# Kernel optimization log

Measured on AMD Instinct MI355X. Metric: run time of the kernel, lower is better.

## Reference

```python
import jax, jax.numpy as jnp
jax.config.update("jax_enable_x64", True)  # original computes in float64
import numpy as np

ALPHA = 0.01  # init kwarg


def setup_inputs() -> dict:
    key = jax.random.key(0)
    x = jax.random.normal(key, (8, 8192, 512), dtype=jnp.float32)
    return {"x": x}


def reference(x):
    # x: [B, T, C]
    _, t, _ = x.shape
    # powers = flip(arange(t)) = [t-1, t-2, ..., 0]
    powers = jnp.arange(t - 1, -1, -1, dtype=jnp.float64)
    base = jnp.power(1.0 - ALPHA, powers)          # (1-alpha)^(t-1-i), [T]
    divisor = base.reshape(1, t, 1)                # [1, T, 1]
    weights = base.at[1:].multiply(ALPHA).reshape(1, t, 1)
    out = jnp.cumsum(x.astype(jnp.float64) * weights, axis=1) / divisor
    return out.astype(x.dtype)
```

## Files before the change

### kernel.cpp

```cpp
#include <hip/hip_runtime.h>
#include <math.h>


namespace {
constexpr int B = 8;
constexpr int T = 8192;
constexpr int C = 512;
constexpr float ALPHA = 0.01f;
constexpr float DECAY = 1.0f - ALPHA;
constexpr int S4 = C / 4;
constexpr int TPB = S4;
constexpr int CHUNK = 64;
constexpr int K = T / CHUNK;
constexpr int W = 32;

typedef float f32x4 __attribute__((ext_vector_type(4)));

__device__ __forceinline__ void ema_step(float4& y, const float4 v) {
    y.x = DECAY * y.x + ALPHA * v.x;
    y.y = DECAY * y.y + ALPHA * v.y;
    y.z = DECAY * y.z + ALPHA * v.z;
    y.w = DECAY * y.w + ALPHA * v.w;
}
}

__global__ __launch_bounds__(TPB) void ema_ends(const float* __restrict__ x,
                                                float* __restrict__ ends) {
    const int k = blockIdx.x;
    const int b = blockIdx.y;
    const int tid = threadIdx.x;
    const float4* xp = reinterpret_cast<const float4*>(x) +
                       (size_t)(b * T + k * CHUNK) * S4 + tid;
    float4 y;
    if (k == 0) {
        y = xp[0];
    } else {
        y = make_float4(0.f, 0.f, 0.f, 0.f);
    }
#pragma unroll 8
    for (int t = 0; t < CHUNK; ++t) {
        float4 v = xp[(size_t)t * S4];
        ema_step(y, v);
    }
    reinterpret_cast<float4*>(ends)[(size_t)(b * K + k) * S4 + tid] = y;
}

__global__ __launch_bounds__(TPB) void ema_fold_apply(const float* __restrict__ x,
                                                      const float* __restrict__ ends,
                                                      float* __restrict__ out,
                                                      float dC) {
    const int k = blockIdx.x;
    const int b = blockIdx.y;
    const int tid = threadIdx.x;
    const size_t base4 = (size_t)(b * T + k * CHUNK) * S4 + tid;
    const float4* xp = reinterpret_cast<const float4*>(x) + base4;
    float4* op = reinterpret_cast<float4*>(out) + base4;

    float4 y;
    if (k == 0) {
        y = xp[0];
    } else {
        y = make_float4(0.f, 0.f, 0.f, 0.f);
        const float4* ep = reinterpret_cast<const float4*>(ends) +
                           (size_t)b * K * S4 + tid;
        int m0 = k - W;
        if (m0 < 0) m0 = 0;
#pragma unroll 8
        for (int m = m0; m < k; ++m) {
            float4 e = ep[(size_t)m * S4];
            y.x = dC * y.x + e.x;
            y.y = dC * y.y + e.y;
            y.z = dC * y.z + e.z;
            y.w = dC * y.w + e.w;
        }
    }
#pragma unroll 8
    for (int t = 0; t < CHUNK; ++t) {
        float4 v = xp[(size_t)t * S4];
        ema_step(y, v);
        __builtin_nontemporal_store(*reinterpret_cast<const f32x4*>(&y),
                                    reinterpret_cast<f32x4*>(op + (size_t)t * S4));
    }
}

__global__ __launch_bounds__(TPB) void ema_seq_kernel(const float* __restrict__ x,
                                                      float* __restrict__ out) {
    const int b = blockIdx.x;
    const int tid = threadIdx.x;
    const float4* xp = reinterpret_cast<const float4*>(x) + (size_t)b * T * S4 + tid;
    float4* op = reinterpret_cast<float4*>(out) + (size_t)b * T * S4 + tid;
    float4 y = xp[0];
    for (int t = 0; t < T; ++t) {
        float4 v = xp[(size_t)t * S4];
        ema_step(y, v);
        op[(size_t)t * S4] = y;
    }
}

extern "C" void kernel_launch(void* const* d_in, const int* in_sizes, int n_in,
                              void* d_out, int out_size, void* d_ws, size_t ws_size,
                              hipStream_t stream) {
    (void)in_sizes; (void)n_in; (void)out_size;
    const float* x = reinterpret_cast<const float*>(d_in[0]);
    float* out = reinterpret_cast<float*>(d_out);

    const size_t need = (size_t)B * K * C * sizeof(float);
    if (ws_size >= need) {
        float* ends = reinterpret_cast<float*>(d_ws);
        const float dC = (float)pow((double)DECAY, (double)CHUNK);
        ema_ends<<<dim3(K, B), dim3(TPB), 0, stream>>>(x, ends);
        ema_fold_apply<<<dim3(K, B), dim3(TPB), 0, stream>>>(x, ends, out, dC);
    } else {
        ema_seq_kernel<<<dim3(B), dim3(TPB), 0, stream>>>(x, out);
    }
}
```

Before: 250.8 us.

## Fuse chunk-ends and fold-apply into single pass with inter-block flag waits

```diff
diff --git a/kernel.cpp b/kernel.cpp
--- a/kernel.cpp
+++ b/kernel.cpp
@@ -13,6 +13,7 @@
 constexpr int CHUNK = 64;
 constexpr int K = T / CHUNK;
 constexpr int W = 32;
+constexpr int NFLAGS = K * B;
 
 typedef float f32x4 __attribute__((ext_vector_type(4)));
 
@@ -24,13 +25,21 @@
 }
 }
 
-__global__ __launch_bounds__(TPB) void ema_ends(const float* __restrict__ x,
-                                                float* __restrict__ ends) {
+__global__ __launch_bounds__(1024) void ema_zero_flags(unsigned int* flags) {
+    flags[threadIdx.x] = 0u;
+}
+
+__global__ __launch_bounds__(TPB) void ema_onepass(const float* __restrict__ x,
+                                                   float* __restrict__ out,
+                                                   float* __restrict__ ends,
+                                                   unsigned int* __restrict__ flags,
+                                                   float dC) {
     const int k = blockIdx.x;
     const int b = blockIdx.y;
     const int tid = threadIdx.x;
-    const float4* xp = reinterpret_cast<const float4*>(x) +
-                       (size_t)(b * T + k * CHUNK) * S4 + tid;
+    const size_t base4 = (size_t)(b * T + k * CHUNK) * S4 + tid;
+    const float4* xp = reinterpret_cast<const float4*>(x) + base4;
+
     float4 y;
     if (k == 0) {
         y = xp[0];
@@ -42,38 +51,42 @@
         float4 v = xp[(size_t)t * S4];
         ema_step(y, v);
     }
-    reinterpret_cast<float4*>(ends)[(size_t)(b * K + k) * S4 + tid] = y;
-}
 
-__global__ __launch_bounds__(TPB) void ema_fold_apply(const float* __restrict__ x,
-                                                      const float* __restrict__ ends,
-                                                      float* __restrict__ out,
-                                                      float dC) {
-    const int k = blockIdx.x;
-    const int b = blockIdx.y;
-    const int tid = threadIdx.x;
-    const size_t base4 = (size_t)(b * T + k * CHUNK) * S4 + tid;
-    const float4* xp = reinterpret_cast<const float4*>(x) + base4;
-    float4* op = reinterpret_cast<float4*>(out) + base4;
+    float4* ep = reinterpret_cast<float4*>(ends) + (size_t)b * K * S4;
+    ep[(size_t)k * S4 + tid] = y;
+    __threadfence();
+    __syncthreads();
+    if (tid == 0) {
+        __hip_atomic_store(&flags[b * K + k], 1u,
+                           __ATOMIC_RELEASE, __HIP_MEMORY_SCOPE_AGENT);
+    }
 
-    float4 y;
     if (k == 0) {
         y = xp[0];
     } else {
+        const int m0 = (k > W) ? (k - W) : 0;
+        const int cnt = k - m0;
+        if (tid < cnt) {
+            while (__hip_atomic_load(&flags[b * K + m0 + tid],
+                                     __ATOMIC_RELAXED,
+                                     __HIP_MEMORY_SCOPE_AGENT) == 0u) {
+                __builtin_amdgcn_s_sleep(8);
+            }
+        }
+        __syncthreads();
+        __threadfence();
         y = make_float4(0.f, 0.f, 0.f, 0.f);
-        const float4* ep = reinterpret_cast<const float4*>(ends) +
-                           (size_t)b * K * S4 + tid;
-        int m0 = k - W;
-        if (m0 < 0) m0 = 0;
 #pragma unroll 8
         for (int m = m0; m < k; ++m) {
-            float4 e = ep[(size_t)m * S4];
+            float4 e = ep[(size_t)m * S4 + tid];
             y.x = dC * y.x + e.x;
             y.y = dC * y.y + e.y;
             y.z = dC * y.z + e.z;
             y.w = dC * y.w + e.w;
         }
     }
+
+    float4* op = reinterpret_cast<float4*>(out) + base4;
 #pragma unroll 8
     for (int t = 0; t < CHUNK; ++t) {
         float4 v = xp[(size_t)t * S4];
@@ -104,12 +117,16 @@
     const float* x = reinterpret_cast<const float*>(d_in[0]);
     float* out = reinterpret_cast<float*>(d_out);
 
-    const size_t need = (size_t)B * K * C * sizeof(float);
+    const size_t ends_bytes = (size_t)B * K * C * sizeof(float);
+    const size_t need = ends_bytes + NFLAGS * sizeof(unsigned int);
+
     if (ws_size >= need) {
         float* ends = reinterpret_cast<float*>(d_ws);
+        unsigned int* flags =
+            reinterpret_cast<unsigned int*>(reinterpret_cast<char*>(d_ws) + ends_bytes);
         const float dC = (float)pow((double)DECAY, (double)CHUNK);
-        ema_ends<<<dim3(K, B), dim3(TPB), 0, stream>>>(x, ends);
-        ema_fold_apply<<<dim3(K, B), dim3(TPB), 0, stream>>>(x, ends, out, dC);
+        ema_zero_flags<<<dim3(1), dim3(NFLAGS), 0, stream>>>(flags);
+        ema_onepass<<<dim3(K, B), dim3(TPB), 0, stream>>>(x, out, ends, flags, dC);
     } else {
         ema_seq_kernel<<<dim3(B), dim3(TPB), 0, stream>>>(x, out);
     }
```

After: 363.9 us. 1.45x slower.

## Break EMA dependency chains with weighted sums and double-buffered loads

Applied to the files above, without the earlier changes.

```diff
diff --git a/kernel.cpp b/kernel.cpp
--- a/kernel.cpp
+++ b/kernel.cpp
@@ -12,15 +12,28 @@
 constexpr int TPB = S4;
 constexpr int CHUNK = 64;
 constexpr int K = T / CHUNK;
-constexpr int W = 32;
+constexpr int W = 16;
 
 typedef float f32x4 __attribute__((ext_vector_type(4)));
+
+constexpr float dpow(int n) {
+    float r = 1.0f;
+    for (int i = 0; i < n; ++i) r *= DECAY;
+    return r;
+}
 
 __device__ __forceinline__ void ema_step(float4& y, const float4 v) {
     y.x = DECAY * y.x + ALPHA * v.x;
     y.y = DECAY * y.y + ALPHA * v.y;
     y.z = DECAY * y.z + ALPHA * v.z;
     y.w = DECAY * y.w + ALPHA * v.w;
+}
+
+__device__ __forceinline__ void wsum(float4& a, const float w, const float4 v) {
+    a.x += w * v.x;
+    a.y += w * v.y;
+    a.z += w * v.z;
+    a.w += w * v.w;
 }
 }
 
@@ -31,42 +44,74 @@
     const int tid = threadIdx.x;
     const float4* xp = reinterpret_cast<const float4*>(x) +
                        (size_t)(b * T + k * CHUNK) * S4 + tid;
+    float4 a0 = make_float4(0.f, 0.f, 0.f, 0.f);
+    float4 a1 = a0, a2 = a0, a3 = a0;
+    float4 x0;
+#pragma unroll
+    for (int t = 0; t < CHUNK; t += 4) {
+        float4 v0 = xp[(size_t)(t + 0) * S4];
+        float4 v1 = xp[(size_t)(t + 1) * S4];
+        float4 v2 = xp[(size_t)(t + 2) * S4];
+        float4 v3 = xp[(size_t)(t + 3) * S4];
+        if (t == 0) x0 = v0;
+        wsum(a0, ALPHA * dpow(CHUNK - 1 - (t + 0)), v0);
+        wsum(a1, ALPHA * dpow(CHUNK - 1 - (t + 1)), v1);
+        wsum(a2, ALPHA * dpow(CHUNK - 1 - (t + 2)), v2);
+        wsum(a3, ALPHA * dpow(CHUNK - 1 - (t + 3)), v3);
+    }
     float4 y;
+    y.x = (a0.x + a1.x) + (a2.x + a3.x);
+    y.y = (a0.y + a1.y) + (a2.y + a3.y);
+    y.z = (a0.z + a1.z) + (a2.z + a3.z);
+    y.w = (a0.w + a1.w) + (a2.w + a3.w);
     if (k == 0) {
-        y = xp[0];
-    } else {
-        y = make_float4(0.f, 0.f, 0.f, 0.f);
-    }
-#pragma unroll 8
-    for (int t = 0; t < CHUNK; ++t) {
-        float4 v = xp[(size_t)t * S4];
-        ema_step(y, v);
+        constexpr float e0 = (1.0f - ALPHA) * dpow(CHUNK - 1);
+        y.x += e0 * x0.x; y.y += e0 * x0.y; y.z += e0 * x0.z; y.w += e0 * x0.w;
     }
     reinterpret_cast<float4*>(ends)[(size_t)(b * K + k) * S4 + tid] = y;
 }
 
-__global__ __launch_bounds__(TPB) void ema_fold_apply(const float* __restrict__ x,
-                                                      const float* __restrict__ ends,
-                                                      float* __restrict__ out,
-                                                      float dC) {
+__global__ __launch_bounds__(TPB) void ema_apply(const float* __restrict__ x,
+                                                 const float* __restrict__ ends,
+                                                 float* __restrict__ out) {
     const int k = blockIdx.x;
     const int b = blockIdx.y;
     const int tid = threadIdx.x;
     const size_t base4 = (size_t)(b * T + k * CHUNK) * S4 + tid;
     const float4* xp = reinterpret_cast<const float4*>(x) + base4;
     float4* op = reinterpret_cast<float4*>(out) + base4;
+    const float4* ep = reinterpret_cast<const float4*>(ends) +
+                       (size_t)b * K * S4 + tid;
+
+    float4 buf[2][8];
+#pragma unroll
+    for (int i = 0; i < 8; ++i) buf[0][i] = xp[(size_t)i * S4];
 
     float4 y;
     if (k == 0) {
-        y = xp[0];
+        y = buf[0][0];
+    } else if (k > W) {
+        float4 c0 = make_float4(0.f, 0.f, 0.f, 0.f);
+        float4 c1 = c0, c2 = c0, c3 = c0;
+#pragma unroll
+        for (int j = 0; j < W; j += 4) {
+            float4 e0 = ep[(size_t)(k - 1 - (j + 0)) * S4];
+            float4 e1 = ep[(size_t)(k - 1 - (j + 1)) * S4];
+            float4 e2 = ep[(size_t)(k - 1 - (j + 2)) * S4];
+            float4 e3 = ep[(size_t)(k - 1 - (j + 3)) * S4];
+            wsum(c0, dpow(CHUNK * (j + 0)), e0);
+            wsum(c1, dpow(CHUNK * (j + 1)), e1);
+            wsum(c2, dpow(CHUNK * (j + 2)), e2);
+            wsum(c3, dpow(CHUNK * (j + 3)), e3);
+        }
+        y.x = (c0.x + c1.x) + (c2.x + c3.x);
+        y.y = (c0.y + c1.y) + (c2.y + c3.y);
+        y.z = (c0.z + c1.z) + (c2.z + c3.z);
+        y.w = (c0.w + c1.w) + (c2.w + c3.w);
     } else {
+        constexpr float dC = dpow(CHUNK);
         y = make_float4(0.f, 0.f, 0.f, 0.f);
-        const float4* ep = reinterpret_cast<const float4*>(ends) +
-                           (size_t)b * K * S4 + tid;
-        int m0 = k - W;
-        if (m0 < 0) m0 = 0;
-#pragma unroll 8
-        for (int m = m0; m < k; ++m) {
+        for (int m = 0; m < k; ++m) {
             float4 e = ep[(size_t)m * S4];
             y.x = dC * y.x + e.x;
             y.y = dC * y.y + e.y;
@@ -74,12 +119,22 @@
             y.w = dC * y.w + e.w;
         }
     }
-#pragma unroll 8
-    for (int t = 0; t < CHUNK; ++t) {
-        float4 v = xp[(size_t)t * S4];
-        ema_step(y, v);
-        __builtin_nontemporal_store(*reinterpret_cast<const f32x4*>(&y),
-                                    reinterpret_cast<f32x4*>(op + (size_t)t * S4));
+
+#pragma unroll
+    for (int g = 0; g < 8; ++g) {
+        const int cur = g & 1, nxt = cur ^ 1;
+        if (g < 7) {
+#pragma unroll
+            for (int i = 0; i < 8; ++i)
+                buf[nxt][i] = xp[(size_t)((g + 1) * 8 + i) * S4];
+        }
+#pragma unroll
+        for (int i = 0; i < 8; ++i) {
+            ema_step(y, buf[cur][i]);
+            __builtin_nontemporal_store(
+                *reinterpret_cast<const f32x4*>(&y),
+                reinterpret_cast<f32x4*>(op + (size_t)(g * 8 + i) * S4));
+        }
     }
 }
 
@@ -107,9 +162,8 @@
     const size_t need = (size_t)B * K * C * sizeof(float);
     if (ws_size >= need) {
         float* ends = reinterpret_cast<float*>(d_ws);
-        const float dC = (float)pow((double)DECAY, (double)CHUNK);
         ema_ends<<<dim3(K, B), dim3(TPB), 0, stream>>>(x, ends);
-        ema_fold_apply<<<dim3(K, B), dim3(TPB), 0, stream>>>(x, ends, out, dC);
+        ema_apply<<<dim3(K, B), dim3(TPB), 0, stream>>>(x, ends, out);
     } else {
         ema_seq_kernel<<<dim3(B), dim3(TPB), 0, stream>>>(x, out);
     }
```

After: 262.4 us. 1.05x slower.

## Fuse chunk-end and apply passes into one cooperative kernel with grid sync

Applied to the files above, without the earlier changes.

```diff
diff --git a/kernel.cpp b/kernel.cpp
--- a/kernel.cpp
+++ b/kernel.cpp
@@ -1,6 +1,9 @@
 #include <hip/hip_runtime.h>
+#include <hip/hip_cooperative_groups.h>
 #include <math.h>
 
+
+namespace cg = cooperative_groups;
 
 namespace {
 constexpr int B = 8;
@@ -12,9 +15,15 @@
 constexpr int TPB = S4;
 constexpr int CHUNK = 64;
 constexpr int K = T / CHUNK;
-constexpr int W = 32;
+constexpr int W = 16;
 
 typedef float f32x4 __attribute__((ext_vector_type(4)));
+
+constexpr float dpow(int n) {
+    float r = 1.0f;
+    for (int i = 0; i < n; ++i) r *= DECAY;
+    return r;
+}
 
 __device__ __forceinline__ void ema_step(float4& y, const float4 v) {
     y.x = DECAY * y.x + ALPHA * v.x;
@@ -22,7 +31,84 @@
     y.z = DECAY * y.z + ALPHA * v.z;
     y.w = DECAY * y.w + ALPHA * v.w;
 }
-}
+
+__device__ __forceinline__ void wsum(float4& a, const float w, const float4 v) {
+    a.x += w * v.x;
+    a.y += w * v.y;
+    a.z += w * v.z;
+    a.w += w * v.w;
+}
+}
+
+__global__ __launch_bounds__(TPB) void ema_fused(const float* __restrict__ x,
+                                                 float* __restrict__ out,
+                                                 float* __restrict__ ends) {
+    const int k = blockIdx.x;
+    const int b = blockIdx.y;
+    const int tid = threadIdx.x;
+    const size_t base4 = (size_t)(b * T + k * CHUNK) * S4 + tid;
+    const float4* xp = reinterpret_cast<const float4*>(x) + base4;
+    float4* ep = reinterpret_cast<float4*>(ends) + (size_t)b * K * S4 + tid;
+
+    float4 y;
+    if (k == 0) {
+        y = xp[0];
+    } else {
+        y = make_float4(0.f, 0.f, 0.f, 0.f);
+    }
+#pragma unroll 8
+    for (int t = 0; t < CHUNK; ++t) {
+        float4 v = xp[(size_t)t * S4];
+        ema_step(y, v);
+    }
+    ep[(size_t)k * S4] = y;
+
+    __threadfence();
+    cg::this_grid().sync();
+    __threadfence();
+
+    if (k == 0) {
+        y = xp[0];
+    } else if (k > W) {
+        float4 c0 = make_float4(0.f, 0.f, 0.f, 0.f);
+        float4 c1 = c0, c2 = c0, c3 = c0;
+#pragma unroll
+        for (int j = 0; j < W; j += 4) {
+            float4 e0 = ep[(size_t)(k - 1 - (j + 0)) * S4];
+            float4 e1 = ep[(size_t)(k - 1 - (j + 1)) * S4];
+            float4 e2 = ep[(size_t)(k - 1 - (j + 2)) * S4];
+            float4 e3 = ep[(size_t)(k - 1 - (j + 3)) * S4];
+            wsum(c0, dpow(CHUNK * (j + 0)), e0);
+            wsum(c1, dpow(CHUNK * (j + 1)), e1);
+            wsum(c2, dpow(CHUNK * (j + 2)), e2);
+            wsum(c3, dpow(CHUNK * (j + 3)), e3);
+        }
+        y.x = (c0.x + c1.x) + (c2.x + c3.x);
+        y.y = (c0.y + c1.y) + (c2.y + c3.y);
+        y.z = (c0.z + c1.z) + (c2.z + c3.z);
+        y.w = (c0.w + c1.w) + (c2.w + c3.w);
+    } else {
+        constexpr float dC = dpow(CHUNK);
+        y = make_float4(0.f, 0.f, 0.f, 0.f);
+        for (int m = 0; m < k; ++m) {
+            float4 e = ep[(size_t)m * S4];
+            y.x = dC * y.x + e.x;
+            y.y = dC * y.y + e.y;
+            y.z = dC * y.z + e.z;
+            y.w = dC * y.w + e.w;
+        }
+    }
+
+    float4* op = reinterpret_cast<float4*>(out) + base4;
+#pragma unroll 8
+    for (int t = 0; t < CHUNK; ++t) {
+        float4 v = xp[(size_t)t * S4];
+        ema_step(y, v);
+        __builtin_nontemporal_store(*reinterpret_cast<const f32x4*>(&y),
+                                    reinterpret_cast<f32x4*>(op + (size_t)t * S4));
+    }
+}
+
 
 __global__ __launch_bounds__(TPB) void ema_ends(const float* __restrict__ x,
                                                 float* __restrict__ ends) {
@@ -45,28 +131,42 @@
     reinterpret_cast<float4*>(ends)[(size_t)(b * K + k) * S4 + tid] = y;
 }
 
-__global__ __launch_bounds__(TPB) void ema_fold_apply(const float* __restrict__ x,
-                                                      const float* __restrict__ ends,
-                                                      float* __restrict__ out,
-                                                      float dC) {
+__global__ __launch_bounds__(TPB) void ema_apply(const float* __restrict__ x,
+                                                 const float* __restrict__ ends,
+                                                 float* __restrict__ out) {
     const int k = blockIdx.x;
     const int b = blockIdx.y;
     const int tid = threadIdx.x;
     const size_t base4 = (size_t)(b * T + k * CHUNK) * S4 + tid;
     const float4* xp = reinterpret_cast<const float4*>(x) + base4;
     float4* op = reinterpret_cast<float4*>(out) + base4;
-
+    const float4* ep = reinterpret_cast<const float4*>(ends) +
+                       (size_t)b * K * S4 + tid;
     float4 y;
     if (k == 0) {
         y = xp[0];
-    } else {
-        y = make_float4(0.f, 0.f, 0.f, 0.f);
-        const float4* ep = reinterpret_cast<const float4*>(ends) +
-                           (size_t)b * K * S4 + tid;
-        int m0 = k - W;
-        if (m0 < 0) m0 = 0;
-#pragma unroll 8
-        for (int m = m0; m < k; ++m) {
+    } else if (k > W) {
+        float4 c0 = make_float4(0.f, 0.f, 0.f, 0.f);
+        float4 c1 = c0, c2 = c0, c3 = c0;
+#pragma unroll
+        for (int j = 0; j < W; j += 4) {
+            float4 e0 = ep[(size_t)(k - 1 - (j + 0)) * S4];
+            float4 e1 = ep[(size_t)(k - 1 - (j + 1)) * S4];
+            float4 e2 = ep[(size_t)(k - 1 - (j + 2)) * S4];
+            float4 e3 = ep[(size_t)(k - 1 - (j + 3)) * S4];
+            wsum(c0, dpow(CHUNK * (j + 0)), e0);
+            wsum(c1, dpow(CHUNK * (j + 1)), e1);
+            wsum(c2, dpow(CHUNK * (j + 2)), e2);
+            wsum(c3, dpow(CHUNK * (j + 3)), e3);
+        }
+        y.x = (c0.x + c1.x) + (c2.x + c3.x);
+        y.y = (c0.y + c1.y) + (c2.y + c3.y);
+        y.z = (c0.z + c1.z) + (c2.z + c3.z);
+        y.w = (c0.w + c1.w) + (c2.w + c3.w);
+    } else {
+        constexpr float dC = dpow(CHUNK);
+        y = make_float4(0.f, 0.f, 0.f, 0.f);
+        for (int m = 0; m < k; ++m) {
             float4 e = ep[(size_t)m * S4];
             y.x = dC * y.x + e.x;
             y.y = dC * y.y + e.y;
@@ -107,9 +207,14 @@
     const size_t need = (size_t)B * K * C * sizeof(float);
     if (ws_size >= need) {
         float* ends = reinterpret_cast<float*>(d_ws);
-        const float dC = (float)pow((double)DECAY, (double)CHUNK);
-        ema_ends<<<dim3(K, B), dim3(TPB), 0, stream>>>(x, ends);
-        ema_fold_apply<<<dim3(K, B), dim3(TPB), 0, stream>>>(x, ends, out, dC);
+        void* args[] = {(void*)&x, (void*)&out, (void*)&ends};
+        hipError_t err = hipLaunchCooperativeKernel(
+            reinterpret_cast<const void*>(ema_fused),
+            dim3(K, B), dim3(TPB), args, 0, stream);
+        if (err != hipSuccess) {
+            ema_ends<<<dim3(K, B), dim3(TPB), 0, stream>>>(x, ends);
+            ema_apply<<<dim3(K, B), dim3(TPB), 0, stream>>>(x, ends, out);
+        }
     } else {
         ema_seq_kernel<<<dim3(B), dim3(TPB), 0, stream>>>(x, out);
     }
```

After: 433.8 us. 73.0% more time.
